# Performance work log

Measured on AMD Instinct MI355X. Metric: run time of the kernel, lower is better.

Reference implementation:

```python
import jax, jax.numpy as jnp
import numpy as np

IN_NC = 32
OUT_NC = 32
HIDDEN = 192  # in_nc * expand_ratio(6)
KS = 3
EPS = 1e-5


def setup_inputs() -> dict:
    key = jax.random.key(0)
    k1, k2 = jax.random.split(key)
    b, h, w = 8, 128, 128
    fh = fw = 8
    hyper = IN_NC * HIDDEN + HIDDEN * KS * KS + HIDDEN * OUT_NC  # 14016
    return {
        "x": jax.random.normal(k1, (b, IN_NC, h, w), jnp.float32),
        "s": jax.random.normal(k2, (b, hyper, fh, fw), jnp.float32),
        "g1": jnp.ones((HIDDEN,), jnp.float32),
        "b1": jnp.zeros((HIDDEN,), jnp.float32),
        "g2": jnp.ones((HIDDEN,), jnp.float32),
        "b2": jnp.zeros((HIDDEN,), jnp.float32),
        "g3": jnp.ones((OUT_NC,), jnp.float32),
        "b3": jnp.zeros((OUT_NC,), jnp.float32),
    }


def _bn(x, gamma, beta):
    # x: [P, H, W, C]; training-mode BatchNorm2d over (P, H, W) per channel
    mean = jnp.mean(x, axis=(0, 1, 2))
    var = jnp.var(x, axis=(0, 1, 2))  # biased, matches torch normalization
    return (x - mean) * jax.lax.rsqrt(var + EPS) * gamma + beta


def _relu6(x):
    return jnp.clip(x, 0.0, 6.0)


def _forward(x, s, g1, b1, g2, b2, g3, b3):
    b, c, h, w = x.shape
    fh, fw = s.shape[-2], s.shape[-1]
    ph, pw = h // fh, w // fw
    kh, kw = ph + 2, pw + 2  # padding (1,1)

    # reflect-pad then unfold into per-patch tiles [P, kh, kw, c]
    xp = jnp.pad(x, ((0, 0), (0, 0), (1, 1), (1, 1)), mode="reflect")
    xp = xp.transpose(0, 2, 3, 1)  # [b, h+2, w+2, c]
    ih = jnp.arange(fh)[:, None] * ph + jnp.arange(kh)[None, :]  # [fh, kh]
    iw = jnp.arange(fw)[:, None] * pw + jnp.arange(kw)[None, :]  # [fw, kw]
    t = xp[:, ih]            # [b, fh, kh, w+2, c]
    t = t[:, :, :, iw]       # [b, fh, kh, fw, kw, c]
    patches = t.transpose(0, 1, 3, 2, 4, 5).reshape(b * fh * fw, kh, kw, c)

    # per-patch hypernet weights
    wt = s.transpose(0, 2, 3, 1).reshape(b * fh * fw, -1)  # [P, hyper]
    r1 = IN_NC * HIDDEN
    r2 = r1 + HIDDEN * KS * KS
    w1 = wt[:, :r1].reshape(-1, HIDDEN, IN_NC)          # pointwise expand
    w2 = wt[:, r1:r2].reshape(-1, HIDDEN, KS, KS)        # depthwise 3x3
    w3 = wt[:, r2:].reshape(-1, OUT_NC, HIDDEN)          # pointwise project

    # 1x1 expand + BN + ReLU6
    x1 = jnp.einsum("pijc,poc->pijo", patches, w1)       # [P, kh, kw, hidden]
    x1 = _relu6(_bn(x1, g1, b1))

    # depthwise 3x3 (valid, stride 1) + BN + ReLU6
    ii = jnp.arange(ph)[:, None] + jnp.arange(KS)[None, :]
    jj = jnp.arange(pw)[:, None] + jnp.arange(KS)[None, :]
    win = x1[:, ii]          # [P, ph, 3, kw, hidden]
    win = win[:, :, :, jj]   # [P, ph, 3, pw, 3, hidden]
    x2 = jnp.einsum("piujvc,pcuv->pijc", win, w2)        # [P, ph, pw, hidden]
    x2 = _relu6(_bn(x2, g2, b2))

    # 1x1 project + BN
    x3 = jnp.einsum("pijc,poc->pijo", x2, w3)            # [P, ph, pw, out]
    x3 = _bn(x3, g3, b3)

    out = x3.reshape(b, fh, fw, ph, pw, OUT_NC)
    out = out.transpose(0, 5, 1, 3, 2, 4).reshape(b, OUT_NC, h, w)
    return x + out  # use_res_connect: stride==1 and in_nc==out_nc


def reference(x, s, g1, b1, g2, b2, g3, b3):
    return _forward(x, s, g1, b1, g2, b2, g3, b3)
```

## Files before the change

### kernel.cpp

```cpp
#include <hip/hip_runtime.h>

#define EPS 1e-5f

namespace {
constexpr int HYPER = 14016;
constexpr int HID   = 192;
constexpr int A1    = 324;
constexpr int A2    = 256;
constexpr int P_TOT = 512;
constexpr int W1SZ  = 6144;
constexpr int WT2SZ = 7872;
constexpr int R3OFF = 1728;

constexpr size_t WB1_B = 0;
constexpr size_t WT2_B = 6291456;
constexpr size_t X2_B  = WT2_B + 16121856;
constexpr size_t X3_B  = X2_B + 50331648;
constexpr size_t SUM_B = X3_B + 8388608;
}

typedef __attribute__((ext_vector_type(8))) short bf16x8;
typedef __attribute__((ext_vector_type(4))) float f32x4;

__device__ __forceinline__ float relu6f(float v) { return fminf(fmaxf(v, 0.f), 6.f); }

__device__ __forceinline__ float bf2f(unsigned int h) {
  return __uint_as_float(h << 16);
}
__device__ __forceinline__ unsigned short f2bf(float f) {
  unsigned int u = __float_as_uint(f);
  return (unsigned short)((u + 0x7FFFu + ((u >> 16) & 1u)) >> 16);
}

__device__ __host__ __forceinline__ int afrag_slot(int o, int c) {
  return (o >> 4) * 512 + (c >> 3) * 128 + (o & 15) * 8 + (c & 7);
}

__global__ __launch_bounds__(256) void k0_transpose(const float* __restrict__ s,
                                                    unsigned short* __restrict__ wb1,
                                                    float* __restrict__ wt2) {
  __shared__ float tile[64][65];
  const int blk = blockIdx.x;
  const int b  = blk / 219;
  const int kt = blk - b * 219;
  const int k0 = kt * 64;
  const int t  = threadIdx.x;
  {
    const int f  = t & 63;
    const int kr = t >> 6;
    const float* sp = s + ((size_t)b * HYPER + k0 + kr) * 64 + f;
#pragma unroll
    for (int kk = 0; kk < 16; kk++)
      tile[kr + kk * 4][f] = sp[(size_t)kk * 4 * 64];
  }
  __syncthreads();
  {
    const int kk = t & 63;
    const int fr = t >> 6;
    if (kt < 96) {
      const int k = k0 + kk;
      const int o = k >> 5, c = k & 31;
      const int slot = afrag_slot(o, c);
      unsigned short* wp = wb1 + ((size_t)b * 64 + fr) * W1SZ + slot;
#pragma unroll
      for (int ff = 0; ff < 16; ff++)
        wp[(size_t)ff * 4 * W1SZ] = f2bf(tile[kk][fr + ff * 4]);
    } else {
      float* wp = wt2 + ((size_t)b * 64 + fr) * WT2SZ + (k0 - W1SZ) + kk;
#pragma unroll
      for (int ff = 0; ff < 16; ff++)
        wp[(size_t)ff * 4 * WT2SZ] = tile[kk][fr + ff * 4];
    }
  }
}

__global__ __launch_bounds__(256) void k1_stats(const float* __restrict__ x,
                                                const unsigned short* __restrict__ wb1,
                                                float* __restrict__ sums) {
  __shared__ __align__(16) unsigned short pL[21 * 512];
  __shared__ float stat[384];
  const int p  = blockIdx.x;
  const int b  = p >> 6;
  const int fi = (p >> 3) & 7;
  const int fj = p & 7;
  const int t  = threadIdx.x;

  for (int i = t; i < 384; i += 256) stat[i] = 0.f;

  const int row0 = fi * 16 - 1, col0 = fj * 16 - 1;
  const float* xb = x + (size_t)b * 32 * 128 * 128;
  for (int idx = t; idx < 32 * A1; idx += 256) {
    int c  = idx / A1;
    int ij = idx - c * A1;
    int ii = ij / 18;
    int jj = ij - ii * 18;
    int r  = row0 + ii; r  = (r  < 0) ? 1 : (r  > 127) ? 126 : r;
    int cl = col0 + jj; cl = (cl < 0) ? 1 : (cl > 127) ? 126 : cl;
    int slot = ((ij >> 4) * 4 + (c >> 3)) * 128 + (ij & 15) * 8 + (c & 7);
    pL[slot] = f2bf(xb[((size_t)c * 128 + r) * 128 + cl]);
  }
  __syncthreads();

  const int lane = t & 63;
  const int wv   = t >> 6;
  const int m16  = lane & 15;
  const int quad = lane >> 4;
  const unsigned short* wbp = wb1 + (size_t)p * W1SZ;

  for (int oi = 0; oi < 3; oi++) {
    const int ot = wv + oi * 4;
    bf16x8 a = *(const bf16x8*)(wbp + ot * 512 + lane * 8);
    float sacc[4] = {0.f, 0.f, 0.f, 0.f};
    float qacc[4] = {0.f, 0.f, 0.f, 0.f};
    for (int jt = 0; jt < 21; jt++) {
      bf16x8 bb = *(const bf16x8*)&pL[jt * 512 + lane * 8];
      f32x4 d = __builtin_amdgcn_mfma_f32_16x16x32_bf16(a, bb, (f32x4){0.f, 0.f, 0.f, 0.f}, 0, 0, 0);
      const int ij = jt * 16 + m16;
      if (ij < A1) {
#pragma unroll
        for (int r = 0; r < 4; r++) {
          float v = d[r];
          sacc[r] += v;
          qacc[r] = fmaf(v, v, qacc[r]);
        }
      }
    }
#pragma unroll
    for (int r = 0; r < 4; r++) {
      float sv = sacc[r], qv = qacc[r];
#pragma unroll
      for (int msk = 1; msk < 16; msk <<= 1) {
        sv += __shfl_xor(sv, msk, 64);
        qv += __shfl_xor(qv, msk, 64);
      }
      if (m16 == 0) {
        int o = ot * 16 + quad * 4 + r;
        atomicAdd(&stat[o], sv);
        atomicAdd(&stat[192 + o], qv);
      }
    }
  }
  __syncthreads();
  for (int i = t; i < 384; i += 256) atomicAdd(&sums[i], stat[i]);
}

__global__ __launch_bounds__(256) void k2_fused(const float* __restrict__ x,
                                                const unsigned short* __restrict__ wb1,
                                                const float* __restrict__ wt2,
                                                const float* __restrict__ sums,
                                                const float* __restrict__ g1,
                                                const float* __restrict__ b1,
                                                unsigned short* __restrict__ x2,
                                                float* __restrict__ sums2) {
  __shared__ __align__(16) unsigned short pL[21 * 512];
  __shared__ __align__(16) unsigned short xc[16 * 328];
  __shared__ __align__(16) unsigned short x2s[256 * 18];
  __shared__ float w2L[HID * 9];
  __shared__ float sc[HID], sh[HID];
  __shared__ float st2[384];
  const int p  = blockIdx.x;
  const int b  = p >> 6;
  const int fi = (p >> 3) & 7;
  const int fj = p & 7;
  const int t  = threadIdx.x;

  const float inv1 = 1.f / 165888.f;
  for (int c = t; c < HID; c += 256) {
    float m   = sums[c] * inv1;
    float var = sums[192 + c] * inv1 - m * m;
    float scl = g1[c] * rsqrtf(var + EPS);
    sc[c] = scl;
    sh[c] = b1[c] - m * scl;
  }
  for (int i = t; i < 384; i += 256) st2[i] = 0.f;
  {
    const float* wtp = wt2 + (size_t)p * WT2SZ;
    for (int i = t; i < HID * 9; i += 256) w2L[i] = wtp[i];
  }

  const int row0 = fi * 16 - 1, col0 = fj * 16 - 1;
  const float* xb = x + (size_t)b * 32 * 128 * 128;
  for (int idx = t; idx < 32 * A1; idx += 256) {
    int c  = idx / A1;
    int ij = idx - c * A1;
    int ii = ij / 18;
    int jj = ij - ii * 18;
    int r  = row0 + ii; r  = (r  < 0) ? 1 : (r  > 127) ? 126 : r;
    int cl = col0 + jj; cl = (cl < 0) ? 1 : (cl > 127) ? 126 : cl;
    int slot = ((ij >> 4) * 4 + (c >> 3)) * 128 + (ij & 15) * 8 + (c & 7);
    pL[slot] = f2bf(xb[((size_t)c * 128 + r) * 128 + cl]);
  }
  __syncthreads();

  const int lane = t & 63;
  const int wv   = t >> 6;
  const int m16  = lane & 15;
  const int quad = lane >> 4;
  const int ih  = t >> 7;
  const int cdw = (t >> 3) & 15;
  const int jp  = t & 7;
  const unsigned short* wbp = wb1 + (size_t)p * W1SZ;
  unsigned short* x2base = x2 + (size_t)p * 12 * 4096;

  auto conv1 = [&](int rt) {
    bf16x8 a = *(const bf16x8*)(wbp + rt * 512 + lane * 8);
    for (int jt = wv; jt < 21; jt += 4) {
      bf16x8 bb = *(const bf16x8*)&pL[jt * 512 + lane * 8];
      f32x4 d = __builtin_amdgcn_mfma_f32_16x16x32_bf16(a, bb, (f32x4){0.f, 0.f, 0.f, 0.f}, 0, 0, 0);
      const int ij = jt * 16 + m16;
      if (ij < A1) {
#pragma unroll
        for (int r = 0; r < 4; r++) {
          int cl = quad * 4 + r;
          int ch = rt * 16 + cl;
          float v = relu6f(fmaf(d[r], sc[ch], sh[ch]));
          xc[cl * 328 + ij] = f2bf(v);
        }
      }
    }
  };

  conv1(0);
  __syncthreads();

  for (int rt = 0; rt < 12; rt++) {
    {
      const int ch = rt * 16 + cdw;
      float wr[9];
#pragma unroll
      for (int u = 0; u < 9; u++) wr[u] = w2L[ch * 9 + u];
      float a0[8], a1[8];
#pragma unroll
      for (int i = 0; i < 8; i++) { a0[i] = 0.f; a1[i] = 0.f; }
      const unsigned short* xcc = &xc[cdw * 328];
#pragma unroll
      for (int rr = 0; rr < 10; rr++) {
        const int rg = ih * 8 + rr;
        unsigned int d0 = *(const unsigned int*)&xcc[rg * 18 + jp * 2];
        unsigned int d1 = *(const unsigned int*)&xcc[rg * 18 + jp * 2 + 2];
        float v0 = bf2f(d0 & 0xFFFFu), v1 = bf2f(d0 >> 16);
        float v2 = bf2f(d1 & 0xFFFFu), v3 = bf2f(d1 >> 16);
#pragma unroll
        for (int u = 0; u < 3; u++) {
          int il = rr - u;
          if (il >= 0 && il < 8) {
            a0[il] = fmaf(v0, wr[u * 3 + 0], fmaf(v1, wr[u * 3 + 1], fmaf(v2, wr[u * 3 + 2], a0[il])));
            a1[il] = fmaf(v1, wr[u * 3 + 0], fmaf(v2, wr[u * 3 + 1], fmaf(v3, wr[u * 3 + 2], a1[il])));
          }
        }
      }
      float ls = 0.f, lq = 0.f;
#pragma unroll
      for (int il = 0; il < 8; il++) {
        const int ig = ih * 8 + il;
        const int j0 = jp * 2;
        unsigned short h0 = f2bf(a0[il]);
        unsigned short h1 = f2bf(a1[il]);
        float r0 = bf2f(h0), r1 = bf2f(h1);
        ls += r0 + r1;
        lq = fmaf(r0, r0, fmaf(r1, r1, lq));
        x2s[(ig * 16 + j0) * 18 + cdw]     = h0;
        x2s[(ig * 16 + j0 + 1) * 18 + cdw] = h1;
      }
      ls += __shfl_xor(ls, 1, 64); lq += __shfl_xor(lq, 1, 64);
      ls += __shfl_xor(ls, 2, 64); lq += __shfl_xor(lq, 2, 64);
      ls += __shfl_xor(ls, 4, 64); lq += __shfl_xor(lq, 4, 64);
      if (jp == 0) {
        atomicAdd(&st2[ch], ls);
        atomicAdd(&st2[192 + ch], lq);
      }
    }
    __syncthreads();
    {
      unsigned short* dst = x2base + (size_t)rt * 4096;
#pragma unroll
      for (int k = 0; k < 4; k++) {
        int g  = (k * 256 + t) * 4;
        int ij = g >> 4, c0 = g & 15;
        unsigned int v0 = *(const unsigned int*)&x2s[ij * 18 + c0];
        unsigned int v1 = *(const unsigned int*)&x2s[ij * 18 + c0 + 2];
        uint2 v; v.x = v0; v.y = v1;
        *(uint2*)&dst[g] = v;
      }
    }
    if (rt < 11) conv1(rt + 1);
    __syncthreads();
  }
  for (int i = t; i < 384; i += 256) atomicAdd(&sums2[i], st2[i]);
}

__global__ __launch_bounds__(256) void k3_pw2(const unsigned short* __restrict__ x2,
                                              const float* __restrict__ wt2,
                                              const float* __restrict__ sums2,
                                              const float* __restrict__ g2,
                                              const float* __restrict__ b2,
                                              unsigned short* __restrict__ x3,
                                              float* __restrict__ sums3) {
  __shared__ __align__(16) unsigned short wA[12 * 512];
  __shared__ float sc[HID], sh[HID];
  __shared__ float st3[64];
  const int blk  = blockIdx.x;
  const int p    = blk >> 1;
  const int half = blk & 1;
  const int t    = threadIdx.x;
  const float inv = 1.f / 131072.f;
  for (int c = t; c < HID; c += 256) {
    float m   = sums2[c] * inv;
    float var = sums2[192 + c] * inv - m * m;
    float scl = g2[c] * rsqrtf(var + EPS);
    sc[c] = scl;
    sh[c] = b2[c] - m * scl;
  }
  if (t < 64) st3[t] = 0.f;
  const float* w3p = wt2 + (size_t)p * WT2SZ + R3OFF;
  for (int idx = t; idx < 32 * 48; idx += 256) {
    int o  = idx / 48;
    int c4 = idx - o * 48;
    float4 v = *(const float4*)&w3p[o * HID + c4 * 4];
    int slot = ((o >> 4) * 6 + (c4 >> 3)) * 512 + ((((c4 >> 1) & 3) * 16) + (o & 15)) * 8 + (c4 & 1) * 4;
    ushort4 u;
    u.x = f2bf(v.x); u.y = f2bf(v.y); u.z = f2bf(v.z); u.w = f2bf(v.w);
    *(ushort4*)&wA[slot] = u;
  }
  __syncthreads();
  const int lane = t & 63;
  const int wv   = t >> 6;
  const int m16  = lane & 15;
  const int kg   = lane >> 4;
  bf16x8 aF[2][6];
#pragma unroll
  for (int ot = 0; ot < 2; ot++)
#pragma unroll
    for (int ks = 0; ks < 6; ks++)
      aF[ot][ks] = *(const bf16x8*)&wA[(ot * 6 + ks) * 512 + lane * 8];
  const unsigned short* x2p = x2 + (size_t)p * 12 * 4096;
  f32x4 acc[2][2];
#pragma unroll
  for (int it = 0; it < 2; it++)
#pragma unroll
    for (int ot = 0; ot < 2; ot++)
#pragma unroll
      for (int r = 0; r < 4; r++) acc[it][ot][r] = 0.f;
#pragma unroll
  for (int it = 0; it < 2; it++) {
    const int ijt = half * 8 + wv + it * 4;
    const int ij  = ijt * 16 + m16;
    const unsigned short* brow = x2p + (size_t)(kg >> 1) * 4096 + (size_t)ij * 16 + (kg & 1) * 8;
#pragma unroll
    for (int ks = 0; ks < 6; ks++) {
      ushort4 u0 = *(const ushort4*)&brow[ks * 8192];
      ushort4 u1 = *(const ushort4*)&brow[ks * 8192 + 4];
      const float* scp = &sc[ks * 32 + kg * 8];
      const float* shp = &sh[ks * 32 + kg * 8];
      unsigned short uu[8] = {u0.x, u0.y, u0.z, u0.w, u1.x, u1.y, u1.z, u1.w};
      bf16x8 bb;
#pragma unroll
      for (int j = 0; j < 8; j++) {
        float y = relu6f(fmaf(bf2f(uu[j]), scp[j], shp[j]));
        bb[j] = (short)f2bf(y);
      }
      acc[it][0] = __builtin_amdgcn_mfma_f32_16x16x32_bf16(aF[0][ks], bb, acc[it][0], 0, 0, 0);
      acc[it][1] = __builtin_amdgcn_mfma_f32_16x16x32_bf16(aF[1][ks], bb, acc[it][1], 0, 0, 0);
    }
  }
  unsigned short* x3p = x3 + (size_t)p * 32 * A2;
  float sacc[2][4] = {{0.f}}, qacc[2][4] = {{0.f}};
#pragma unroll
  for (int it = 0; it < 2; it++) {
    const int ijt = half * 8 + wv + it * 4;
#pragma unroll
    for (int ot = 0; ot < 2; ot++) {
#pragma unroll
      for (int r = 0; r < 4; r++) {
        unsigned short h = f2bf(acc[it][ot][r]);
        float v = bf2f(h);
        x3p[(size_t)(ot * 16 + kg * 4 + r) * A2 + ijt * 16 + m16] = h;
        sacc[ot][r] += v;
        qacc[ot][r] = fmaf(v, v, qacc[ot][r]);
      }
    }
  }
#pragma unroll
  for (int ot = 0; ot < 2; ot++)
#pragma unroll
    for (int r = 0; r < 4; r++) {
      float sv = sacc[ot][r], qv = qacc[ot][r];
#pragma unroll
      for (int msk = 1; msk < 16; msk <<= 1) {
        sv += __shfl_xor(sv, msk, 64);
        qv += __shfl_xor(qv, msk, 64);
      }
      if (m16 == 0) {
        int o = ot * 16 + kg * 4 + r;
        atomicAdd(&st3[o], sv);
        atomicAdd(&st3[32 + o], qv);
      }
    }
  __syncthreads();
  if (t < 64) atomicAdd(&sums3[t], st3[t]);
}

__global__ __launch_bounds__(256) void k4_out(const float* __restrict__ x,
                                              const unsigned short* __restrict__ x3,
                                              const float* __restrict__ sums3,
                                              const float* __restrict__ g3,
                                              const float* __restrict__ b3,
                                              float* __restrict__ out) {
  const int idx4 = blockIdx.x * 256 + threadIdx.x;
  const int w4 = idx4 & 31;
  int tmp = idx4 >> 5;
  const int h = tmp & 127; tmp >>= 7;
  const int o = tmp & 31;
  const int b = tmp >> 5;
  const int fi = h >> 4, i = h & 15;
  const int fj = w4 >> 2;
  const int j0 = (w4 & 3) * 4;
  const int p   = b * 64 + fi * 8 + fj;
  const int ij0 = i * 16 + j0;
  const float inv = 1.f / 131072.f;
  float m   = sums3[o] * inv;
  float var = sums3[32 + o] * inv - m * m;
  float sv  = g3[o] * rsqrtf(var + EPS);
  float shv = b3[o] - m * sv;
  float4 xv = *(const float4*)&x[(size_t)idx4 * 4];
  ushort4 u = *(const ushort4*)&x3[((size_t)p * 32 + o) * A2 + ij0];
  float4 r;
  r.x = fmaf(bf2f(u.x), sv, shv) + xv.x;
  r.y = fmaf(bf2f(u.y), sv, shv) + xv.y;
  r.z = fmaf(bf2f(u.z), sv, shv) + xv.z;
  r.w = fmaf(bf2f(u.w), sv, shv) + xv.w;
  *(float4*)&out[(size_t)idx4 * 4] = r;
}

extern "C" void kernel_launch(void* const* d_in, const int* in_sizes, int n_in,
                              void* d_out, int out_size, void* d_ws, size_t ws_size,
                              hipStream_t stream) {
  const float* x  = (const float*)d_in[0];
  const float* s  = (const float*)d_in[1];
  const float* g1 = (const float*)d_in[2];
  const float* b1 = (const float*)d_in[3];
  const float* g2 = (const float*)d_in[4];
  const float* b2 = (const float*)d_in[5];
  const float* g3 = (const float*)d_in[6];
  const float* b3 = (const float*)d_in[7];
  char* base = (char*)d_ws;
  unsigned short* wb1  = (unsigned short*)(base + WB1_B);
  float*          wt2  = (float*)(base + WT2_B);
  unsigned short* x2   = (unsigned short*)(base + X2_B);
  unsigned short* x3   = (unsigned short*)(base + X3_B);
  float*          sums = (float*)(base + SUM_B);
  float* out = (float*)d_out;

  hipMemsetAsync(sums, 0, 832 * sizeof(float), stream);
  k0_transpose<<<8 * 219, 256, 0, stream>>>(s, wb1, wt2);
  k1_stats<<<P_TOT, 256, 0, stream>>>(x, wb1, sums);
  k2_fused<<<P_TOT, 256, 0, stream>>>(x, wb1, wt2, sums, g1, b1, x2, sums + 384);
  k3_pw2<<<1024, 256, 0, stream>>>(x2, wt2, sums + 384, g2, b2, x3, sums + 768);
  k4_out<<<4096, 256, 0, stream>>>(x, x3, sums + 768, g3, b3, out);
}
```

Baseline: 221.0 us.

## Split fused expand/depthwise kernel across channel tiles for more blocks

The fused expand+depthwise kernel now launches one block per (patch, 16-channel tile) instead of one block per patch looping over 12 channel tiles. This raises the grid from 512 to 6144 blocks, which is meant to give better occupancy and load balance across CUs. The cost is that every block reloads and converts the whole 32-channel input patch from global memory, so input traffic and patch staging work are repeated twelve times. Each block handles only its own slices of the BN scale, the depthwise weights and the statistics.

```diff
diff --git a/kernel.cpp b/kernel.cpp
--- a/kernel.cpp
+++ b/kernel.cpp
@@ -155,27 +155,30 @@
   __shared__ __align__(16) unsigned short pL[21 * 512];
   __shared__ __align__(16) unsigned short xc[16 * 328];
   __shared__ __align__(16) unsigned short x2s[256 * 18];
-  __shared__ float w2L[HID * 9];
-  __shared__ float sc[HID], sh[HID];
-  __shared__ float st2[384];
-  const int p  = blockIdx.x;
+  __shared__ float w2L[16 * 9];
+  __shared__ float scc[16], shc[16];
+  __shared__ float st2[32];
+  const int blk = blockIdx.x;
+  const int p   = blk / 12;
+  const int rt  = blk - p * 12;
   const int b  = p >> 6;
   const int fi = (p >> 3) & 7;
   const int fj = p & 7;
   const int t  = threadIdx.x;
 
   const float inv1 = 1.f / 165888.f;
-  for (int c = t; c < HID; c += 256) {
+  if (t < 16) {
+    int c = rt * 16 + t;
     float m   = sums[c] * inv1;
     float var = sums[192 + c] * inv1 - m * m;
     float scl = g1[c] * rsqrtf(var + EPS);
-    sc[c] = scl;
-    sh[c] = b1[c] - m * scl;
-  }
-  for (int i = t; i < 384; i += 256) st2[i] = 0.f;
-  {
-    const float* wtp = wt2 + (size_t)p * WT2SZ;
-    for (int i = t; i < HID * 9; i += 256) w2L[i] = wtp[i];
+    scc[t] = scl;
+    shc[t] = b1[c] - m * scl;
+  }
+  if (t < 32) st2[t] = 0.f;
+  if (t >= 32 && t < 32 + 144) {
+    int i = t - 32;
+    w2L[i] = wt2[(size_t)p * WT2SZ + rt * 144 + i];
   }
 
   const int row0 = fi * 16 - 1, col0 = fj * 16 - 1;
@@ -196,14 +199,9 @@
   const int wv   = t >> 6;
   const int m16  = lane & 15;
   const int quad = lane >> 4;
-  const int ih  = t >> 7;
-  const int cdw = (t >> 3) & 15;
-  const int jp  = t & 7;
-  const unsigned short* wbp = wb1 + (size_t)p * W1SZ;
-  unsigned short* x2base = x2 + (size_t)p * 12 * 4096;
-
-  auto conv1 = [&](int rt) {
-    bf16x8 a = *(const bf16x8*)(wbp + rt * 512 + lane * 8);
+
+  {
+    bf16x8 a = *(const bf16x8*)(wb1 + (size_t)p * W1SZ + rt * 512 + lane * 8);
     for (int jt = wv; jt < 21; jt += 4) {
       bf16x8 bb = *(const bf16x8*)&pL[jt * 512 + lane * 8];
       f32x4 d = __builtin_amdgcn_mfma_f32_16x16x32_bf16(a, bb, (f32x4){0.f, 0.f, 0.f, 0.f}, 0, 0, 0);
@@ -212,81 +210,78 @@
 #pragma unroll
         for (int r = 0; r < 4; r++) {
           int cl = quad * 4 + r;
-          int ch = rt * 16 + cl;
-          float v = relu6f(fmaf(d[r], sc[ch], sh[ch]));
+          float v = relu6f(fmaf(d[r], scc[cl], shc[cl]));
           xc[cl * 328 + ij] = f2bf(v);
         }
       }
     }
-  };
-
-  conv1(0);
-  __syncthreads();
-
-  for (int rt = 0; rt < 12; rt++) {
-    {
-      const int ch = rt * 16 + cdw;
-      float wr[9];
-#pragma unroll
-      for (int u = 0; u < 9; u++) wr[u] = w2L[ch * 9 + u];
-      float a0[8], a1[8];
-#pragma unroll
-      for (int i = 0; i < 8; i++) { a0[i] = 0.f; a1[i] = 0.f; }
-      const unsigned short* xcc = &xc[cdw * 328];
-#pragma unroll
-      for (int rr = 0; rr < 10; rr++) {
-        const int rg = ih * 8 + rr;
-        unsigned int d0 = *(const unsigned int*)&xcc[rg * 18 + jp * 2];
-        unsigned int d1 = *(const unsigned int*)&xcc[rg * 18 + jp * 2 + 2];
-        float v0 = bf2f(d0 & 0xFFFFu), v1 = bf2f(d0 >> 16);
-        float v2 = bf2f(d1 & 0xFFFFu), v3 = bf2f(d1 >> 16);
-#pragma unroll
-        for (int u = 0; u < 3; u++) {
-          int il = rr - u;
-          if (il >= 0 && il < 8) {
-            a0[il] = fmaf(v0, wr[u * 3 + 0], fmaf(v1, wr[u * 3 + 1], fmaf(v2, wr[u * 3 + 2], a0[il])));
-            a1[il] = fmaf(v1, wr[u * 3 + 0], fmaf(v2, wr[u * 3 + 1], fmaf(v3, wr[u * 3 + 2], a1[il])));
-          }
+  }
+  __syncthreads();
+
+  {
+    const int ih  = t >> 7;
+    const int cdw = (t >> 3) & 15;
+    const int jp  = t & 7;
+    float wr[9];
+#pragma unroll
+    for (int u = 0; u < 9; u++) wr[u] = w2L[cdw * 9 + u];
+    float a0[8], a1[8];
+#pragma unroll
+    for (int i = 0; i < 8; i++) { a0[i] = 0.f; a1[i] = 0.f; }
+    const unsigned short* xcc = &xc[cdw * 328];
+#pragma unroll
+    for (int rr = 0; rr < 10; rr++) {
+      const int rg = ih * 8 + rr;
+      unsigned int d0 = *(const unsigned int*)&xcc[rg * 18 + jp * 2];
+      unsigned int d1 = *(const unsigned int*)&xcc[rg * 18 + jp * 2 + 2];
+      float v0 = bf2f(d0 & 0xFFFFu), v1 = bf2f(d0 >> 16);
+      float v2 = bf2f(d1 & 0xFFFFu), v3 = bf2f(d1 >> 16);
+#pragma unroll
+      for (int u = 0; u < 3; u++) {
+        int il = rr - u;
+        if (il >= 0 && il < 8) {
+          a0[il] = fmaf(v0, wr[u * 3 + 0], fmaf(v1, wr[u * 3 + 1], fmaf(v2, wr[u * 3 + 2], a0[il])));
+          a1[il] = fmaf(v1, wr[u * 3 + 0], fmaf(v2, wr[u * 3 + 1], fmaf(v3, wr[u * 3 + 2], a1[il])));
         }
       }
-      float ls = 0.f, lq = 0.f;
-#pragma unroll
-      for (int il = 0; il < 8; il++) {
-        const int ig = ih * 8 + il;
-        const int j0 = jp * 2;
-        unsigned short h0 = f2bf(a0[il]);
-        unsigned short h1 = f2bf(a1[il]);
-        float r0 = bf2f(h0), r1 = bf2f(h1);
-        ls += r0 + r1;
-        lq = fmaf(r0, r0, fmaf(r1, r1, lq));
-        x2s[(ig * 16 + j0) * 18 + cdw]     = h0;
-        x2s[(ig * 16 + j0 + 1) * 18 + cdw] = h1;
-      }
-      ls += __shfl_xor(ls, 1, 64); lq += __shfl_xor(lq, 1, 64);
-      ls += __shfl_xor(ls, 2, 64); lq += __shfl_xor(lq, 2, 64);
-      ls += __shfl_xor(ls, 4, 64); lq += __shfl_xor(lq, 4, 64);
-      if (jp == 0) {
-        atomicAdd(&st2[ch], ls);
-        atomicAdd(&st2[192 + ch], lq);
-      }
-    }
-    __syncthreads();
-    {
-      unsigned short* dst = x2base + (size_t)rt * 4096;
-#pragma unroll
-      for (int k = 0; k < 4; k++) {
-        int g  = (k * 256 + t) * 4;
-        int ij = g >> 4, c0 = g & 15;
-        unsigned int v0 = *(const unsigned int*)&x2s[ij * 18 + c0];
-        unsigned int v1 = *(const unsigned int*)&x2s[ij * 18 + c0 + 2];
-        uint2 v; v.x = v0; v.y = v1;
-        *(uint2*)&dst[g] = v;
-      }
-    }
-    if (rt < 11) conv1(rt + 1);
-    __syncthreads();
-  }
-  for (int i = t; i < 384; i += 256) atomicAdd(&sums2[i], st2[i]);
+    }
+    float ls = 0.f, lq = 0.f;
+#pragma unroll
+    for (int il = 0; il < 8; il++) {
+      const int ig = ih * 8 + il;
+      const int j0 = jp * 2;
+      unsigned short h0 = f2bf(a0[il]);
+      unsigned short h1 = f2bf(a1[il]);
+      float r0 = bf2f(h0), r1 = bf2f(h1);
+      ls += r0 + r1;
+      lq = fmaf(r0, r0, fmaf(r1, r1, lq));
+      x2s[(ig * 16 + j0) * 18 + cdw]     = h0;
+      x2s[(ig * 16 + j0 + 1) * 18 + cdw] = h1;
+    }
+    ls += __shfl_xor(ls, 1, 64); lq += __shfl_xor(lq, 1, 64);
+    ls += __shfl_xor(ls, 2, 64); lq += __shfl_xor(lq, 2, 64);
+    ls += __shfl_xor(ls, 4, 64); lq += __shfl_xor(lq, 4, 64);
+    if (jp == 0) {
+      atomicAdd(&st2[cdw], ls);
+      atomicAdd(&st2[16 + cdw], lq);
+    }
+  }
+  __syncthreads();
+
+  {
+    unsigned short* dst = x2 + (size_t)p * 12 * 4096 + (size_t)rt * 4096;
+#pragma unroll
+    for (int k = 0; k < 4; k++) {
+      int g  = (k * 256 + t) * 4;
+      int ij = g >> 4, c0 = g & 15;
+      unsigned int v0 = *(const unsigned int*)&x2s[ij * 18 + c0];
+      unsigned int v1 = *(const unsigned int*)&x2s[ij * 18 + c0 + 2];
+      uint2 v; v.x = v0; v.y = v1;
+      *(uint2*)&dst[g] = v;
+    }
+  }
+  if (t < 16)      atomicAdd(&sums2[rt * 16 + t], st2[t]);
+  else if (t < 32) atomicAdd(&sums2[192 + rt * 16 + (t - 16)], st2[t]);
 }
 
 __global__ __launch_bounds__(256) void k3_pw2(const unsigned short* __restrict__ x2,
@@ -454,7 +449,7 @@
   hipMemsetAsync(sums, 0, 832 * sizeof(float), stream);
   k0_transpose<<<8 * 219, 256, 0, stream>>>(s, wb1, wt2);
   k1_stats<<<P_TOT, 256, 0, stream>>>(x, wb1, sums);
-  k2_fused<<<P_TOT, 256, 0, stream>>>(x, wb1, wt2, sums, g1, b1, x2, sums + 384);
+  k2_fused<<<P_TOT * 12, 256, 0, stream>>>(x, wb1, wt2, sums, g1, b1, x2, sums + 384);
   k3_pw2<<<1024, 256, 0, stream>>>(x2, wt2, sums + 384, g2, b2, x3, sums + 768);
   k4_out<<<4096, 256, 0, stream>>>(x, x3, sums + 768, g3, b3, out);
 }
```

Measured after the change: 273.6 us. 23.8% more time.
